# Performance work log

Hardware: AMD Instinct MI355X
Metric: run time of the kernel (lower is better)

## Reference

```python
import jax, jax.numpy as jnp
import numpy as np

C_IN = 12
C1 = 128
C2 = 256
K = 9
PAD = K // 2
T = 20
GAIN = 3.0
TAU1 = 1.0
TAU2 = 0.9
TH1 = 0.02
TH2 = 0.02
NUM_CLASSES = 4
B = 64
L = 2048


def _conv1d(x, w, b):
    # x: [B, Cin, L], w: [Cout, Cin, K] -> [B, Cout, L] (same padding)
    y = jax.lax.conv_general_dilated(
        x, w, window_strides=(1,), padding=[(PAD, PAD)],
        dimension_numbers=('NCH', 'OIH', 'NCH'))
    return y + b[None, :, None]


def setup_inputs() -> dict:
    key = jax.random.key(0)
    ks = jax.random.split(key, 7)
    x = jax.random.normal(ks[0], (B, C_IN, L, T), dtype=jnp.float32)
    fan1 = C_IN * K
    fan2 = C1 * K
    W1 = jax.random.uniform(ks[1], (C1, C_IN, K), jnp.float32, -1, 1) / np.sqrt(fan1)
    b1 = jax.random.uniform(ks[2], (C1,), jnp.float32, -1, 1) / np.sqrt(fan1)
    W2 = jax.random.uniform(ks[3], (C2, C1, K), jnp.float32, -1, 1) / np.sqrt(fan2)
    b2 = jax.random.uniform(ks[4], (C2,), jnp.float32, -1, 1) / np.sqrt(fan2)
    Wfc = jax.random.uniform(ks[5], (NUM_CLASSES, C2), jnp.float32, -1, 1) / np.sqrt(C2)
    bfc = jax.random.uniform(ks[6], (NUM_CLASSES,), jnp.float32, -1, 1) / np.sqrt(C2)
    return {"x": x, "W1": W1, "b1": b1, "W2": W2, "b2": b2, "Wfc": Wfc, "bfc": bfc}


def _lif(v, a, tau, th):
    # v <- v + (a - v)/tau; spike = hard threshold; reset to 0 where spiked
    v = v + (a - v) / tau
    spike = (v >= th).astype(v.dtype)
    v = jnp.where(spike > 0, jnp.zeros_like(v), v)
    return v, spike


def reference(x, W1, b1, W2, b2, Wfc, bfc):
    xt_seq = jnp.moveaxis(x, 3, 0)  # [T, B, Cin, L]
    v1_0 = jnp.zeros((B, C1, L), x.dtype)
    v2_0 = jnp.zeros((B, C2, L), x.dtype)

    def step(carry, xt):
        v1, v2 = carry
        a1 = _conv1d(xt, W1, b1) * GAIN
        v1, s1 = _lif(v1, a1, TAU1, TH1)
        a2 = _conv1d(s1, W2, b2) * GAIN
        v2, s2 = _lif(v2, a2, TAU2, TH2)
        return (v1, v2), s2

    _, spikes = jax.lax.scan(step, (v1_0, v2_0), xt_seq)  # [T, B, C2, L]
    out = jnp.sum(spikes, axis=0) / float(T)  # [B, C2, L]
    pooled = jnp.mean(out, axis=-1)  # AdaptiveAvgPool1d(1) + squeeze -> [B, C2]
    return pooled @ Wfc.T + bfc  # [B, NUM_CLASSES]
```

## Files before the change

### kernel.cpp

```cpp
#include <hip/hip_runtime.h>
#include <hip/hip_bf16.h>


#define NB    64
#define NCIN  12
#define NC1   128
#define NC2   256
#define NT    20
#define NL    2048
#define GAINF 3.0f
#define THF   0.02f
#define W2SCALE 4310.0f

#define BROWS 264
#define BSZ   (BROWS * 128)

typedef __bf16 bf16x8 __attribute__((ext_vector_type(8)));
typedef float  f32x4  __attribute__((ext_vector_type(4)));
typedef int    i32x4  __attribute__((ext_vector_type(4)));

__device__ __forceinline__ unsigned short f2bf(float f) {
  __hip_bfloat16 h = __float2bfloat16(f);
  return __builtin_bit_cast(unsigned short, h);
}

__global__ void snn_wsetup_kernel(const float* __restrict__ W1, const float* __restrict__ W2,
                                  unsigned short* __restrict__ w1t, unsigned char* __restrict__ w2q,
                                  unsigned char* __restrict__ s1p) {
  int idx = blockIdx.x * 256 + threadIdx.x;
  if (idx < 9 * 256 * 128) {
    int c1 = idx & 127;
    int c2 = (idx >> 7) & 255;
    int k  = idx >> 15;
    int c2q = c2 >> 6, c2l = c2 & 63;
    int dst = k * 32768 + c2q * 8192 + (((c2l * 128 + c1)) ^ ((c2l & 7) << 4));
    int q = __float2int_rn(W2[((size_t)c2 * 128 + c1) * 9 + k] * W2SCALE);
    w2q[dst] = (unsigned char)(signed char)q;
  }
  if (idx < 128 * 128) {
    int c1 = idx >> 7, kd = idx & 127;
    float v = 0.f;
    if (kd < 108) {
      int cin = kd / 9, kk = kd - cin * 9;
      v = W1[((size_t)c1 * 12 + cin) * 9 + kk];
    }
    w1t[idx] = f2bf(v);
  }
  if (idx < NB * NT * 8) {
    int bt = idx >> 3, r8 = idx & 7;
    size_t row = (size_t)bt * 2056 + (r8 < 4 ? r8 : 2048 + r8);
    *(uint4*)(s1p + row * 16) = make_uint4(0u, 0u, 0u, 0u);
  }
}

__global__ __launch_bounds__(256, 2) void snn_conv1_kernel(
    const float* __restrict__ x, const float* __restrict__ b1,
    const unsigned short* __restrict__ w1t, unsigned char* __restrict__ s1p) {
  __shared__ alignas(16) unsigned short ldsB[128 * 128];
  __shared__ alignas(16) unsigned short ldsA[128 * 128];
  __shared__ float b1s[128];

  const int tid  = threadIdx.x;
  const int lane = tid & 63;
  const int wv   = tid >> 6;
  const int wm   = wv >> 1, wn = wv & 1;
  const int hi   = lane >> 4, lo = lane & 15;
  const int bid  = blockIdx.x;
  const int t    = bid % 20;
  const int r    = bid / 20;
  const int l0   = (r & 15) << 7;
  const int b    = r >> 4;

  {
    const uint4* gA = (const uint4*)w1t;
#pragma unroll
    for (int i = 0; i < 8; ++i) {
      int idx = tid + i * 256;
      unsigned off = (unsigned)idx * 16u;
      unsigned row = off >> 8;
      *(uint4*)((char*)ldsA + (off ^ ((row & 7u) << 4))) = gA[idx];
    }
  }
  if (tid < 128) b1s[tid] = b1[tid];

  for (int i = tid; i < 128 * 20; i += 256) {
    int n = i / 20, c = 108 + (i - n * 20);
    *(unsigned short*)((char*)ldsB + ((unsigned)(n * 256) + (((unsigned)c * 2u) ^ (((unsigned)n & 7u) << 4)))) = 0;
  }
  for (int e = tid; e < NCIN * 136; e += 256) {
    int cin = e / 136, i = e - cin * 136;
    int l = l0 - 4 + i;
    float xv = 0.f;
    if (l >= 0 && l < NL) xv = x[(((size_t)b * NCIN + cin) * NL + l) * NT + t];
    unsigned short hv = f2bf(xv);
    int kd0 = cin * 9;
#pragma unroll
    for (int k = 0; k < 9; ++k) {
      int n = i - k;
      if (n >= 0 && n < 128) {
        *(unsigned short*)((char*)ldsB + ((unsigned)(n * 256) + (((unsigned)(kd0 + k) * 2u) ^ (((unsigned)n & 7u) << 4)))) = hv;
      }
    }
  }
  __syncthreads();

  f32x4 acc[4][4];
#pragma unroll
  for (int mf = 0; mf < 4; ++mf)
#pragma unroll
    for (int nf = 0; nf < 4; ++nf) acc[mf][nf] = (f32x4){0.f, 0.f, 0.f, 0.f};

#pragma unroll
  for (int chunk = 0; chunk < 4; ++chunk) {
    const unsigned kd2 = (unsigned)(chunk * 32 + hi * 8) * 2u;
    bf16x8 af[4], bfr[4];
#pragma unroll
    for (int mf = 0; mf < 4; ++mf) {
      int rr = wm * 64 + mf * 16 + lo;
      af[mf] = *(const bf16x8*)((const char*)ldsA + ((unsigned)(rr * 256) + (kd2 ^ (((unsigned)rr & 7u) << 4))));
    }
#pragma unroll
    for (int nf = 0; nf < 4; ++nf) {
      int rr = wn * 64 + nf * 16 + lo;
      bfr[nf] = *(const bf16x8*)((const char*)ldsB + ((unsigned)(rr * 256) + (kd2 ^ (((unsigned)rr & 7u) << 4))));
    }
#pragma unroll
    for (int mf = 0; mf < 4; ++mf)
#pragma unroll
      for (int nf = 0; nf < 4; ++nf)
        acc[mf][nf] = __builtin_amdgcn_mfma_f32_16x16x32_bf16(af[mf], bfr[nf], acc[mf][nf], 0, 0, 0);
  }
  __syncthreads();

  unsigned char* ldsP = (unsigned char*)ldsB;
#pragma unroll
  for (int mf = 0; mf < 4; ++mf) {
    int c1b = wm * 64 + mf * 16 + hi * 4;
#pragma unroll
    for (int nf = 0; nf < 4; ++nf) {
      int lrow = wn * 64 + nf * 16 + lo;
      unsigned n4 = 0;
      n4 |= (GAINF * (acc[mf][nf][0] + b1s[c1b + 0]) >= THF) ? 1u : 0u;
      n4 |= (GAINF * (acc[mf][nf][1] + b1s[c1b + 1]) >= THF) ? 2u : 0u;
      n4 |= (GAINF * (acc[mf][nf][2] + b1s[c1b + 2]) >= THF) ? 4u : 0u;
      n4 |= (GAINF * (acc[mf][nf][3] + b1s[c1b + 3]) >= THF) ? 8u : 0u;
      unsigned p = (unsigned)__shfl_xor((int)n4, 16);
      if ((hi & 1) == 0) {
        ldsP[lrow * 16 + (wm * 8 + mf * 2 + (hi >> 1))] = (unsigned char)(n4 | (p << 4));
      }
    }
  }
  __syncthreads();

  if (tid < 128) {
    uint4 v = *(const uint4*)(ldsP + tid * 16);
    *(uint4*)(s1p + ((size_t)(b * 20 + t) * 2056 + 4 + l0 + tid) * 16) = v;
  }
}

__device__ __forceinline__ void expand_store(unsigned char* buf, int n, int h, uint2 bits) {
  unsigned swz = (unsigned)(n & 7) << 4;
  char* rowp = (char*)buf + n * 128;
#pragma unroll
  for (int q = 0; q < 4; ++q) {
    unsigned src = (q < 2) ? bits.x : bits.y;
    int sh = (q & 1) * 16;
    uint4 w;
    w.x = (((src >> (sh + 0)) & 15u) * 0x204081u) & 0x01010101u;
    w.y = (((src >> (sh + 4)) & 15u) * 0x204081u) & 0x01010101u;
    w.z = (((src >> (sh + 8)) & 15u) * 0x204081u) & 0x01010101u;
    w.w = (((src >> (sh + 12)) & 15u) * 0x204081u) & 0x01010101u;
    *(uint4*)(rowp + (((unsigned)(h * 64 + q * 16)) ^ swz)) = w;
  }
}

__global__ __attribute__((amdgpu_flat_work_group_size(512, 512), amdgpu_waves_per_eu(2, 2)))
void snn_conv2_kernel(const unsigned char* __restrict__ s1p, const unsigned char* __restrict__ w2q,
                      const float* __restrict__ b2, float* __restrict__ counts) {
  __shared__ alignas(16) unsigned char ldsW[9 * 8192];
  __shared__ alignas(16) unsigned char ldsBy[2 * BSZ];

  const int tid  = threadIdx.x;
  const int lane = tid & 63;
  const int wv   = tid >> 6;
  const int hi   = lane >> 4, lo = lane & 15;
  const int bid  = blockIdx.x;
  const int b    = bid >> 5;
  const int r5b  = bid & 31;
  const int c2q  = r5b >> 3;
  const int l0   = (r5b & 7) << 8;

#pragma unroll
  for (int tp = 0; tp < 9; ++tp) {
    __builtin_amdgcn_global_load_lds(
        (const __attribute__((address_space(1))) void*)(w2q + (size_t)tp * 32768 + (size_t)c2q * 8192 + wv * 1024 + lane * 16),
        (__attribute__((address_space(3))) void*)(ldsW + tp * 8192 + wv * 1024), 16, 0, 0);
  }

  float gb2[4][4];
#pragma unroll
  for (int mf = 0; mf < 4; ++mf)
#pragma unroll
    for (int j = 0; j < 4; ++j)
      gb2[mf][j] = GAINF * b2[c2q * 64 + mf * 16 + hi * 4 + j];

  f32x4 v2s[4][2];
  int cnt[4][4];
#pragma unroll
  for (int mf = 0; mf < 4; ++mf) {
#pragma unroll
    for (int nf = 0; nf < 2; ++nf) v2s[mf][nf] = (f32x4){0.f, 0.f, 0.f, 0.f};
#pragma unroll
    for (int j = 0; j < 4; ++j) cnt[mf][j] = 0;
  }

  uint2 pA, pB, pC = make_uint2(0u, 0u);
  {
    const unsigned char* spA = s1p + ((size_t)(b * 20 + 0) * 2056 + l0) * 16;
    const unsigned char* spB = s1p + ((size_t)(b * 20 + 1) * 2056 + l0) * 16;
    pA = *(const uint2*)(spA + (size_t)tid * 8);
    pB = (tid < 16) ? *(const uint2*)(spA + (size_t)(512 + tid) * 8)
                    : *(const uint2*)(spB + (size_t)(tid - 16) * 8);
    if (tid < 32) pC = *(const uint2*)(spB + (size_t)(496 + tid) * 8);
  }

  const float it2 = 1.0f / 0.9f;
  const float isc = GAINF / W2SCALE;

  for (int ts = 0; ts < 20; ts += 2) {
    expand_store(ldsBy, tid >> 1, tid & 1, pA);
    if (tid < 16) expand_store(ldsBy, 256 + (tid >> 1), tid & 1, pB);
    else          expand_store(ldsBy + BSZ, (tid - 16) >> 1, (tid - 16) & 1, pB);
    if (tid < 32) expand_store(ldsBy + BSZ, 248 + (tid >> 1), tid & 1, pC);
    __syncthreads();

    if (ts < 18) {
      const unsigned char* snA = s1p + ((size_t)(b * 20 + ts + 2) * 2056 + l0) * 16;
      const unsigned char* snB = s1p + ((size_t)(b * 20 + ts + 3) * 2056 + l0) * 16;
      pA = *(const uint2*)(snA + (size_t)tid * 8);
      pB = (tid < 16) ? *(const uint2*)(snA + (size_t)(512 + tid) * 8)
                      : *(const uint2*)(snB + (size_t)(tid - 16) * 8);
      if (tid < 32) pC = *(const uint2*)(snB + (size_t)(496 + tid) * 8);
    }

    i32x4 acc[4][2][2];
#pragma unroll
    for (int mf = 0; mf < 4; ++mf)
#pragma unroll
      for (int tt = 0; tt < 2; ++tt)
#pragma unroll
        for (int nf = 0; nf < 2; ++nf) acc[mf][tt][nf] = (i32x4){0, 0, 0, 0};

#pragma unroll
    for (int tap = 0; tap < 9; ++tap) {
#pragma unroll
      for (int chunk = 0; chunk < 2; ++chunk) {
        const unsigned ksl = (unsigned)(chunk * 64 + hi * 16);
        i32x4 af[4], bf[2][2];
#pragma unroll
        for (int mf = 0; mf < 4; ++mf) {
          int rr = mf * 16 + lo;
          unsigned off = (unsigned)(rr * 128) + (ksl ^ (((unsigned)rr & 7u) << 4));
          af[mf] = *(const i32x4*)(ldsW + tap * 8192 + off);
        }
#pragma unroll
        for (int nf = 0; nf < 2; ++nf) {
          int rs = wv * 32 + nf * 16 + lo + tap;
          unsigned off = (unsigned)(rs * 128) + (ksl ^ (((unsigned)rs & 7u) << 4));
          bf[0][nf] = *(const i32x4*)(ldsBy + off);
          bf[1][nf] = *(const i32x4*)(ldsBy + BSZ + off);
        }
#pragma unroll
        for (int mf = 0; mf < 4; ++mf)
#pragma unroll
          for (int tt = 0; tt < 2; ++tt)
#pragma unroll
            for (int nf = 0; nf < 2; ++nf)
              acc[mf][tt][nf] = __builtin_amdgcn_mfma_i32_16x16x64_i8(af[mf], bf[tt][nf], acc[mf][tt][nf], 0, 0, 0);
      }
    }

#pragma unroll
    for (int tt = 0; tt < 2; ++tt) {
#pragma unroll
      for (int mf = 0; mf < 4; ++mf) {
#pragma unroll
        for (int nf = 0; nf < 2; ++nf) {
#pragma unroll
          for (int j = 0; j < 4; ++j) {
            float a2 = (float)acc[mf][tt][nf][j] * isc + gb2[mf][j];
            float vo = v2s[mf][nf][j];
            float vn = vo + (a2 - vo) * it2;
            int sp2 = (vn >= THF) ? 1 : 0;
            v2s[mf][nf][j] = sp2 ? 0.f : vn;
            cnt[mf][j] += sp2;
          }
        }
      }
    }

    __syncthreads();
  }

#pragma unroll
  for (int mf = 0; mf < 4; ++mf)
#pragma unroll
    for (int j = 0; j < 4; ++j) {
      int c = cnt[mf][j];
      c += __shfl_xor(c, 1);
      c += __shfl_xor(c, 2);
      c += __shfl_xor(c, 4);
      c += __shfl_xor(c, 8);
      if (lo == 0) {
        int c2g = c2q * 64 + mf * 16 + hi * 4 + j;
        atomicAdd(&counts[b * NC2 + c2g], (float)c);
      }
    }
}

__global__ void snn_fc_kernel(const float* __restrict__ counts, const float* __restrict__ Wfc,
                              const float* __restrict__ bfc, float* __restrict__ out) {
  int tid = threadIdx.x;
  int b = tid >> 2, cls = tid & 3;
  float s = 0.f;
  for (int c = 0; c < 256; ++c) s += counts[b * 256 + c] * Wfc[cls * 256 + c];
  out[tid] = s * (1.0f / ((float)NT * (float)NL)) + bfc[cls];
}

extern "C" void kernel_launch(void* const* d_in, const int* in_sizes, int n_in,
                              void* d_out, int out_size, void* d_ws, size_t ws_size,
                              hipStream_t stream) {
  const float* x   = (const float*)d_in[0];
  const float* W1  = (const float*)d_in[1];
  const float* b1  = (const float*)d_in[2];
  const float* W2  = (const float*)d_in[3];
  const float* b2  = (const float*)d_in[4];
  const float* Wfc = (const float*)d_in[5];
  const float* bfc = (const float*)d_in[6];
  float* out = (float*)d_out;
  char* ws = (char*)d_ws;

  const size_t SZ_S1P = (size_t)NB * NT * 2056 * 16;
  const size_t SZ_W2Q = (size_t)9 * 256 * 128;
  const size_t SZ_W1T = (size_t)128 * 128 * 2;
  const size_t SZ_CNT = (size_t)NB * NC2 * 4;

  const size_t OFF_S1P = 0;
  const size_t OFF_W2Q = OFF_S1P + SZ_S1P;
  const size_t OFF_W1T = OFF_W2Q + SZ_W2Q;
  const size_t OFF_CNT = OFF_W1T + SZ_W1T;
  const size_t NEEDED  = OFF_CNT + SZ_CNT;
  if (ws_size < NEEDED) return;

  unsigned char*  s1p = (unsigned char*)(ws + OFF_S1P);
  unsigned char*  w2q = (unsigned char*)(ws + OFF_W2Q);
  unsigned short* w1t = (unsigned short*)(ws + OFF_W1T);
  float* counts = (float*)(ws + OFF_CNT);

  hipMemsetAsync(counts, 0, SZ_CNT, stream);
  snn_wsetup_kernel<<<1152, 256, 0, stream>>>(W1, W2, w1t, w2q, s1p);
  snn_conv1_kernel<<<NB * 16 * NT, 256, 0, stream>>>(x, b1, w1t, s1p);
  snn_conv2_kernel<<<NB * 4 * 8, 512, 0, stream>>>(s1p, w2q, b2, counts);
  snn_fc_kernel<<<1, 256, 0, stream>>>(counts, Wfc, bfc, out);
}
```

Before: 930.5 us.

## Stream conv2 weights from global in MFMA fragment layout, process four timesteps per tile

Conv2 no longer stages the int8 W2 into LDS. Weights are pre-packed into MFMA A-fragment order and read straight from global/L2 into registers, double-buffered across k-slices. The freed LDS holds four timesteps of expanded spikes for a 128-position tile instead of two timesteps of 256, so each weight fragment is reused over four timesteps and the grid doubles. The cost is repeated global weight loads per block per iteration, which rely on cache hits, plus extra index arithmetic for the staged spike rows.

```diff
diff --git a/kernel.cpp b/kernel.cpp
--- a/kernel.cpp
+++ b/kernel.cpp
@@ -12,8 +12,8 @@
 #define THF   0.02f
 #define W2SCALE 4310.0f
 
-#define BROWS 264
-#define BSZ   (BROWS * 128)
+#define BROWS4 136
+#define BSZ4   (BROWS4 * 128)
 
 typedef __bf16 bf16x8 __attribute__((ext_vector_type(8)));
 typedef float  f32x4  __attribute__((ext_vector_type(4)));
@@ -25,17 +25,19 @@
 }
 
 __global__ void snn_wsetup_kernel(const float* __restrict__ W1, const float* __restrict__ W2,
-                                  unsigned short* __restrict__ w1t, unsigned char* __restrict__ w2q,
+                                  unsigned short* __restrict__ w1t, unsigned char* __restrict__ w2a,
                                   unsigned char* __restrict__ s1p) {
   int idx = blockIdx.x * 256 + threadIdx.x;
   if (idx < 9 * 256 * 128) {
     int c1 = idx & 127;
     int c2 = (idx >> 7) & 255;
     int k  = idx >> 15;
-    int c2q = c2 >> 6, c2l = c2 & 63;
-    int dst = k * 32768 + c2q * 8192 + (((c2l * 128 + c1)) ^ ((c2l & 7) << 4));
+    int c2q = c2 >> 6, rr = c2 & 63;
+    int mf = rr >> 4, lo = rr & 15;
+    int chunk = c1 >> 6, hi = (c1 >> 4) & 3, bb = c1 & 15;
+    int frag = ((c2q * 9 + k) * 2 + chunk) * 4 + mf;
     int q = __float2int_rn(W2[((size_t)c2 * 128 + c1) * 9 + k] * W2SCALE);
-    w2q[dst] = (unsigned char)(signed char)q;
+    w2a[(size_t)frag * 1024 + (hi * 16 + lo) * 16 + bb] = (unsigned char)(signed char)q;
   }
   if (idx < 128 * 128) {
     int c1 = idx >> 7, kd = idx & 127;
@@ -175,27 +177,21 @@
 }
 
 __global__ __attribute__((amdgpu_flat_work_group_size(512, 512), amdgpu_waves_per_eu(2, 2)))
-void snn_conv2_kernel(const unsigned char* __restrict__ s1p, const unsigned char* __restrict__ w2q,
+void snn_conv2_kernel(const unsigned char* __restrict__ s1p, const unsigned char* __restrict__ w2a,
                       const float* __restrict__ b2, float* __restrict__ counts) {
-  __shared__ alignas(16) unsigned char ldsW[9 * 8192];
-  __shared__ alignas(16) unsigned char ldsBy[2 * BSZ];
+  __shared__ alignas(16) unsigned char ldsBy[4 * BSZ4];
 
   const int tid  = threadIdx.x;
   const int lane = tid & 63;
   const int wv   = tid >> 6;
   const int hi   = lane >> 4, lo = lane & 15;
+  const int wl   = wv * 16;
   const int bid  = blockIdx.x;
-  const int b    = bid >> 5;
-  const int r5b  = bid & 31;
-  const int c2q  = r5b >> 3;
-  const int l0   = (r5b & 7) << 8;
-
-#pragma unroll
-  for (int tp = 0; tp < 9; ++tp) {
-    __builtin_amdgcn_global_load_lds(
-        (const __attribute__((address_space(1))) void*)(w2q + (size_t)tp * 32768 + (size_t)c2q * 8192 + wv * 1024 + lane * 16),
-        (__attribute__((address_space(3))) void*)(ldsW + tp * 8192 + wv * 1024), 16, 0, 0);
-  }
+  const int b    = bid >> 6;
+  const int c2q  = (bid >> 4) & 3;
+  const int l0   = (bid & 15) << 7;
+
+  const i32x4* wfrag = (const i32x4*)(w2a + (size_t)c2q * 9 * 2 * 4 * 1024);
 
   float gb2[4][4];
 #pragma unroll
@@ -204,97 +200,102 @@
     for (int j = 0; j < 4; ++j)
       gb2[mf][j] = GAINF * b2[c2q * 64 + mf * 16 + hi * 4 + j];
 
-  f32x4 v2s[4][2];
+  f32x4 v2s[4];
   int cnt[4][4];
 #pragma unroll
   for (int mf = 0; mf < 4; ++mf) {
-#pragma unroll
-    for (int nf = 0; nf < 2; ++nf) v2s[mf][nf] = (f32x4){0.f, 0.f, 0.f, 0.f};
+    v2s[mf] = (f32x4){0.f, 0.f, 0.f, 0.f};
 #pragma unroll
     for (int j = 0; j < 4; ++j) cnt[mf][j] = 0;
   }
 
   uint2 pA, pB, pC = make_uint2(0u, 0u);
   {
-    const unsigned char* spA = s1p + ((size_t)(b * 20 + 0) * 2056 + l0) * 16;
-    const unsigned char* spB = s1p + ((size_t)(b * 20 + 1) * 2056 + l0) * 16;
-    pA = *(const uint2*)(spA + (size_t)tid * 8);
-    pB = (tid < 16) ? *(const uint2*)(spA + (size_t)(512 + tid) * 8)
-                    : *(const uint2*)(spB + (size_t)(tid - 16) * 8);
-    if (tid < 32) pC = *(const uint2*)(spB + (size_t)(496 + tid) * 8);
+    int uA = tid;            int tA = uA / 272, rA = uA - tA * 272;
+    int uB = 512 + tid;      int tB = uB / 272, rB = uB - tB * 272;
+    pA = *(const uint2*)(s1p + ((size_t)(b * 20 + tA) * 2056 + l0 + (rA >> 1)) * 16 + (rA & 1) * 8);
+    pB = *(const uint2*)(s1p + ((size_t)(b * 20 + tB) * 2056 + l0 + (rB >> 1)) * 16 + (rB & 1) * 8);
+    if (tid < 64) {
+      int uC = 1024 + tid;   int tC = uC / 272, rC = uC - tC * 272;
+      pC = *(const uint2*)(s1p + ((size_t)(b * 20 + tC) * 2056 + l0 + (rC >> 1)) * 16 + (rC & 1) * 8);
+    }
   }
 
   const float it2 = 1.0f / 0.9f;
   const float isc = GAINF / W2SCALE;
 
-  for (int ts = 0; ts < 20; ts += 2) {
-    expand_store(ldsBy, tid >> 1, tid & 1, pA);
-    if (tid < 16) expand_store(ldsBy, 256 + (tid >> 1), tid & 1, pB);
-    else          expand_store(ldsBy + BSZ, (tid - 16) >> 1, (tid - 16) & 1, pB);
-    if (tid < 32) expand_store(ldsBy + BSZ, 248 + (tid >> 1), tid & 1, pC);
+  for (int ts = 0; ts < 20; ts += 4) {
+    {
+      int uA = tid;          int tA = uA / 272, rA = uA - tA * 272;
+      int uB = 512 + tid;    int tB = uB / 272, rB = uB - tB * 272;
+      expand_store(ldsBy + tA * BSZ4, rA >> 1, rA & 1, pA);
+      expand_store(ldsBy + tB * BSZ4, rB >> 1, rB & 1, pB);
+      if (tid < 64) {
+        int uC = 1024 + tid; int tC = uC / 272, rC = uC - tC * 272;
+        expand_store(ldsBy + tC * BSZ4, rC >> 1, rC & 1, pC);
+      }
+    }
     __syncthreads();
 
-    if (ts < 18) {
-      const unsigned char* snA = s1p + ((size_t)(b * 20 + ts + 2) * 2056 + l0) * 16;
-      const unsigned char* snB = s1p + ((size_t)(b * 20 + ts + 3) * 2056 + l0) * 16;
-      pA = *(const uint2*)(snA + (size_t)tid * 8);
-      pB = (tid < 16) ? *(const uint2*)(snA + (size_t)(512 + tid) * 8)
-                      : *(const uint2*)(snB + (size_t)(tid - 16) * 8);
-      if (tid < 32) pC = *(const uint2*)(snB + (size_t)(496 + tid) * 8);
-    }
-
-    i32x4 acc[4][2][2];
+    if (ts < 16) {
+      int tsn = ts + 4;
+      int uA = tid;          int tA = uA / 272, rA = uA - tA * 272;
+      int uB = 512 + tid;    int tB = uB / 272, rB = uB - tB * 272;
+      pA = *(const uint2*)(s1p + ((size_t)(b * 20 + tsn + tA) * 2056 + l0 + (rA >> 1)) * 16 + (rA & 1) * 8);
+      pB = *(const uint2*)(s1p + ((size_t)(b * 20 + tsn + tB) * 2056 + l0 + (rB >> 1)) * 16 + (rB & 1) * 8);
+      if (tid < 64) {
+        int uC = 1024 + tid; int tC = uC / 272, rC = uC - tC * 272;
+        pC = *(const uint2*)(s1p + ((size_t)(b * 20 + tsn + tC) * 2056 + l0 + (rC >> 1)) * 16 + (rC & 1) * 8);
+      }
+    }
+
+    i32x4 acc[4][4];
 #pragma unroll
     for (int mf = 0; mf < 4; ++mf)
 #pragma unroll
-      for (int tt = 0; tt < 2; ++tt)
-#pragma unroll
-        for (int nf = 0; nf < 2; ++nf) acc[mf][tt][nf] = (i32x4){0, 0, 0, 0};
-
-#pragma unroll
-    for (int tap = 0; tap < 9; ++tap) {
-#pragma unroll
-      for (int chunk = 0; chunk < 2; ++chunk) {
-        const unsigned ksl = (unsigned)(chunk * 64 + hi * 16);
-        i32x4 af[4], bf[2][2];
-#pragma unroll
-        for (int mf = 0; mf < 4; ++mf) {
-          int rr = mf * 16 + lo;
-          unsigned off = (unsigned)(rr * 128) + (ksl ^ (((unsigned)rr & 7u) << 4));
-          af[mf] = *(const i32x4*)(ldsW + tap * 8192 + off);
-        }
-#pragma unroll
-        for (int nf = 0; nf < 2; ++nf) {
-          int rs = wv * 32 + nf * 16 + lo + tap;
-          unsigned off = (unsigned)(rs * 128) + (ksl ^ (((unsigned)rs & 7u) << 4));
-          bf[0][nf] = *(const i32x4*)(ldsBy + off);
-          bf[1][nf] = *(const i32x4*)(ldsBy + BSZ + off);
-        }
+      for (int tt = 0; tt < 4; ++tt) acc[mf][tt] = (i32x4){0, 0, 0, 0};
+
+    i32x4 afb[2][4];
+#pragma unroll
+    for (int s0 = 0; s0 < 2; ++s0)
+#pragma unroll
+      for (int mf = 0; mf < 4; ++mf)
+        afb[s0][mf] = wfrag[(s0 * 4 + mf) * 64 + lane];
+
+#pragma unroll
+    for (int s = 0; s < 18; ++s) {
+      const int tap = s >> 1;
+      const unsigned ksl = (unsigned)((s & 1) * 64 + hi * 16);
+      const int rs = wl + lo + tap;
+      const unsigned off = (unsigned)(rs * 128) + (ksl ^ (((unsigned)rs & 7u) << 4));
+      i32x4 bfr[4];
+#pragma unroll
+      for (int tt = 0; tt < 4; ++tt)
+        bfr[tt] = *(const i32x4*)(ldsBy + tt * BSZ4 + off);
+#pragma unroll
+      for (int mf = 0; mf < 4; ++mf)
+#pragma unroll
+        for (int tt = 0; tt < 4; ++tt)
+          acc[mf][tt] = __builtin_amdgcn_mfma_i32_16x16x64_i8(afb[s & 1][mf], bfr[tt], acc[mf][tt], 0, 0, 0);
+      if (s < 16) {
 #pragma unroll
         for (int mf = 0; mf < 4; ++mf)
-#pragma unroll
-          for (int tt = 0; tt < 2; ++tt)
-#pragma unroll
-            for (int nf = 0; nf < 2; ++nf)
-              acc[mf][tt][nf] = __builtin_amdgcn_mfma_i32_16x16x64_i8(af[mf], bf[tt][nf], acc[mf][tt][nf], 0, 0, 0);
-      }
-    }
-
-#pragma unroll
-    for (int tt = 0; tt < 2; ++tt) {
+          afb[s & 1][mf] = wfrag[((s + 2) * 4 + mf) * 64 + lane];
+      }
+    }
+
+#pragma unroll
+    for (int tt = 0; tt < 4; ++tt) {
 #pragma unroll
       for (int mf = 0; mf < 4; ++mf) {
 #pragma unroll
-        for (int nf = 0; nf < 2; ++nf) {
-#pragma unroll
-          for (int j = 0; j < 4; ++j) {
-            float a2 = (float)acc[mf][tt][nf][j] * isc + gb2[mf][j];
-            float vo = v2s[mf][nf][j];
-            float vn = vo + (a2 - vo) * it2;
-            int sp2 = (vn >= THF) ? 1 : 0;
-            v2s[mf][nf][j] = sp2 ? 0.f : vn;
-            cnt[mf][j] += sp2;
-          }
+        for (int j = 0; j < 4; ++j) {
+          float a2 = (float)acc[mf][tt][j] * isc + gb2[mf][j];
+          float vo = v2s[mf][j];
+          float vn = vo + (a2 - vo) * it2;
+          int sp2 = (vn >= THF) ? 1 : 0;
+          v2s[mf][j] = sp2 ? 0.f : vn;
+          cnt[mf][j] += sp2;
         }
       }
     }
@@ -341,25 +342,25 @@
   char* ws = (char*)d_ws;
 
   const size_t SZ_S1P = (size_t)NB * NT * 2056 * 16;
-  const size_t SZ_W2Q = (size_t)9 * 256 * 128;
+  const size_t SZ_W2A = (size_t)9 * 256 * 128;
   const size_t SZ_W1T = (size_t)128 * 128 * 2;
   const size_t SZ_CNT = (size_t)NB * NC2 * 4;
 
   const size_t OFF_S1P = 0;
-  const size_t OFF_W2Q = OFF_S1P + SZ_S1P;
-  const size_t OFF_W1T = OFF_W2Q + SZ_W2Q;
+  const size_t OFF_W2A = OFF_S1P + SZ_S1P;
+  const size_t OFF_W1T = OFF_W2A + SZ_W2A;
   const size_t OFF_CNT = OFF_W1T + SZ_W1T;
   const size_t NEEDED  = OFF_CNT + SZ_CNT;
   if (ws_size < NEEDED) return;
 
   unsigned char*  s1p = (unsigned char*)(ws + OFF_S1P);
-  unsigned char*  w2q = (unsigned char*)(ws + OFF_W2Q);
+  unsigned char*  w2a = (unsigned char*)(ws + OFF_W2A);
   unsigned short* w1t = (unsigned short*)(ws + OFF_W1T);
   float* counts = (float*)(ws + OFF_CNT);
 
   hipMemsetAsync(counts, 0, SZ_CNT, stream);
-  snn_wsetup_kernel<<<1152, 256, 0, stream>>>(W1, W2, w1t, w2q, s1p);
+  snn_wsetup_kernel<<<1152, 256, 0, stream>>>(W1, W2, w1t, w2a, s1p);
   snn_conv1_kernel<<<NB * 16 * NT, 256, 0, stream>>>(x, b1, w1t, s1p);
-  snn_conv2_kernel<<<NB * 4 * 8, 512, 0, stream>>>(s1p, w2q, b2, counts);
+  snn_conv2_kernel<<<NB * 4 * 16, 512, 0, stream>>>(s1p, w2a, b2, counts);
   snn_fc_kernel<<<1, 256, 0, stream>>>(counts, Wfc, bfc, out);
 }
```

Result: slower. 2.422 ms (+160.3%).

## Halve conv2 tile length and stream W2 taps through double-buffered LDS

Applied to the files above, without the earlier changes.

The conv2 kernel tile shrinks from 256 to 128 positions per block, and the grid doubles. Instead of keeping all nine W2 tap slices resident in LDS, it double-buffers one tap at a time with async global-to-LDS loads. This cuts LDS use from about 140KB to about 50KB and halves the accumulator registers, so more waves per EU can be resident (waves_per_eu 4) to hide latency. The cost is a barrier after every tap, W2 being re-read from global nine times per timestep pair, and more halo rows relative to the tile size.

```diff
diff --git a/kernel.cpp b/kernel.cpp
--- a/kernel.cpp
+++ b/kernel.cpp
@@ -12,8 +12,8 @@
 #define THF   0.02f
 #define W2SCALE 4310.0f
 
-#define BROWS 264
-#define BSZ   (BROWS * 128)
+#define BROWS2 136
+#define BSZ2   (BROWS2 * 128)
 
 typedef __bf16 bf16x8 __attribute__((ext_vector_type(8)));
 typedef float  f32x4  __attribute__((ext_vector_type(4)));
@@ -174,28 +174,20 @@
   }
 }
 
-__global__ __attribute__((amdgpu_flat_work_group_size(512, 512), amdgpu_waves_per_eu(2, 2)))
+__global__ __attribute__((amdgpu_flat_work_group_size(512, 512), amdgpu_waves_per_eu(4)))
 void snn_conv2_kernel(const unsigned char* __restrict__ s1p, const unsigned char* __restrict__ w2q,
                       const float* __restrict__ b2, float* __restrict__ counts) {
-  __shared__ alignas(16) unsigned char ldsW[9 * 8192];
-  __shared__ alignas(16) unsigned char ldsBy[2 * BSZ];
+  __shared__ alignas(16) unsigned char ldsW[2 * 8192];
+  __shared__ alignas(16) unsigned char ldsBy[2 * BSZ2];
 
   const int tid  = threadIdx.x;
   const int lane = tid & 63;
   const int wv   = tid >> 6;
   const int hi   = lane >> 4, lo = lane & 15;
   const int bid  = blockIdx.x;
-  const int b    = bid >> 5;
-  const int r5b  = bid & 31;
-  const int c2q  = r5b >> 3;
-  const int l0   = (r5b & 7) << 8;
-
-#pragma unroll
-  for (int tp = 0; tp < 9; ++tp) {
-    __builtin_amdgcn_global_load_lds(
-        (const __attribute__((address_space(1))) void*)(w2q + (size_t)tp * 32768 + (size_t)c2q * 8192 + wv * 1024 + lane * 16),
-        (__attribute__((address_space(3))) void*)(ldsW + tp * 8192 + wv * 1024), 16, 0, 0);
-  }
+  const int b    = bid >> 6;
+  const int c2q  = (bid >> 4) & 3;
+  const int l0   = (bid & 15) << 7;
 
   float gb2[4][4];
 #pragma unroll
@@ -204,80 +196,90 @@
     for (int j = 0; j < 4; ++j)
       gb2[mf][j] = GAINF * b2[c2q * 64 + mf * 16 + hi * 4 + j];
 
-  f32x4 v2s[4][2];
+  f32x4 v2s[4];
   int cnt[4][4];
 #pragma unroll
   for (int mf = 0; mf < 4; ++mf) {
-#pragma unroll
-    for (int nf = 0; nf < 2; ++nf) v2s[mf][nf] = (f32x4){0.f, 0.f, 0.f, 0.f};
+    v2s[mf] = (f32x4){0.f, 0.f, 0.f, 0.f};
 #pragma unroll
     for (int j = 0; j < 4; ++j) cnt[mf][j] = 0;
   }
 
-  uint2 pA, pB, pC = make_uint2(0u, 0u);
+  uint2 pA, pB = make_uint2(0u, 0u);
   {
-    const unsigned char* spA = s1p + ((size_t)(b * 20 + 0) * 2056 + l0) * 16;
-    const unsigned char* spB = s1p + ((size_t)(b * 20 + 1) * 2056 + l0) * 16;
-    pA = *(const uint2*)(spA + (size_t)tid * 8);
-    pB = (tid < 16) ? *(const uint2*)(spA + (size_t)(512 + tid) * 8)
-                    : *(const uint2*)(spB + (size_t)(tid - 16) * 8);
-    if (tid < 32) pC = *(const uint2*)(spB + (size_t)(496 + tid) * 8);
-  }
+    pA = *(const uint2*)(s1p + ((size_t)(b * 20 + (tid >= 272)) * 2056 + l0 +
+                                ((tid >= 272 ? tid - 272 : tid) >> 1)) * 16 + (tid & 1) * 8);
+    if (tid < 32) {
+      int u = 512 + tid;
+      pB = *(const uint2*)(s1p + ((size_t)(b * 20 + 1) * 2056 + l0 + ((u - 272) >> 1)) * 16 + (u & 1) * 8);
+    }
+  }
+
+  __builtin_amdgcn_global_load_lds(
+      (const __attribute__((address_space(1))) void*)(w2q + (size_t)c2q * 8192 + wv * 1024 + lane * 16),
+      (__attribute__((address_space(3))) void*)(ldsW + wv * 1024), 16, 0, 0);
+  int cur = 0;
 
   const float it2 = 1.0f / 0.9f;
   const float isc = GAINF / W2SCALE;
 
   for (int ts = 0; ts < 20; ts += 2) {
-    expand_store(ldsBy, tid >> 1, tid & 1, pA);
-    if (tid < 16) expand_store(ldsBy, 256 + (tid >> 1), tid & 1, pB);
-    else          expand_store(ldsBy + BSZ, (tid - 16) >> 1, (tid - 16) & 1, pB);
-    if (tid < 32) expand_store(ldsBy + BSZ, 248 + (tid >> 1), tid & 1, pC);
+    {
+      int tt = (tid >= 272), r = tid - 272 * tt;
+      expand_store(ldsBy + tt * BSZ2, r >> 1, tid & 1, pA);
+      if (tid < 32) expand_store(ldsBy + BSZ2, (512 + tid - 272) >> 1, tid & 1, pB);
+    }
     __syncthreads();
 
     if (ts < 18) {
-      const unsigned char* snA = s1p + ((size_t)(b * 20 + ts + 2) * 2056 + l0) * 16;
-      const unsigned char* snB = s1p + ((size_t)(b * 20 + ts + 3) * 2056 + l0) * 16;
-      pA = *(const uint2*)(snA + (size_t)tid * 8);
-      pB = (tid < 16) ? *(const uint2*)(snA + (size_t)(512 + tid) * 8)
-                      : *(const uint2*)(snB + (size_t)(tid - 16) * 8);
-      if (tid < 32) pC = *(const uint2*)(snB + (size_t)(496 + tid) * 8);
-    }
-
-    i32x4 acc[4][2][2];
+      pA = *(const uint2*)(s1p + ((size_t)(b * 20 + ts + 2 + (tid >= 272)) * 2056 + l0 +
+                                  ((tid >= 272 ? tid - 272 : tid) >> 1)) * 16 + (tid & 1) * 8);
+      if (tid < 32) {
+        int u = 512 + tid;
+        pB = *(const uint2*)(s1p + ((size_t)(b * 20 + ts + 3) * 2056 + l0 + ((u - 272) >> 1)) * 16 + (u & 1) * 8);
+      }
+    }
+
+    i32x4 acc[4][2];
 #pragma unroll
     for (int mf = 0; mf < 4; ++mf)
 #pragma unroll
-      for (int tt = 0; tt < 2; ++tt)
-#pragma unroll
-        for (int nf = 0; nf < 2; ++nf) acc[mf][tt][nf] = (i32x4){0, 0, 0, 0};
+      for (int tt = 0; tt < 2; ++tt) acc[mf][tt] = (i32x4){0, 0, 0, 0};
 
 #pragma unroll
     for (int tap = 0; tap < 9; ++tap) {
+      {
+        int tapn = (tap == 8) ? 0 : tap + 1;
+        __builtin_amdgcn_global_load_lds(
+            (const __attribute__((address_space(1))) void*)(w2q + (size_t)tapn * 32768 + (size_t)c2q * 8192 + wv * 1024 + lane * 16),
+            (__attribute__((address_space(3))) void*)(ldsW + ((cur ^ 1) << 13) + wv * 1024), 16, 0, 0);
+      }
+      const unsigned char* wbuf = ldsW + (cur << 13);
+      __builtin_amdgcn_s_setprio(1);
 #pragma unroll
       for (int chunk = 0; chunk < 2; ++chunk) {
         const unsigned ksl = (unsigned)(chunk * 64 + hi * 16);
-        i32x4 af[4], bf[2][2];
+        i32x4 af[4], bfr[2];
 #pragma unroll
         for (int mf = 0; mf < 4; ++mf) {
           int rr = mf * 16 + lo;
-          unsigned off = (unsigned)(rr * 128) + (ksl ^ (((unsigned)rr & 7u) << 4));
-          af[mf] = *(const i32x4*)(ldsW + tap * 8192 + off);
+          af[mf] = *(const i32x4*)(wbuf + (unsigned)(rr * 128) + (ksl ^ (((unsigned)rr & 7u) << 4)));
         }
-#pragma unroll
-        for (int nf = 0; nf < 2; ++nf) {
-          int rs = wv * 32 + nf * 16 + lo + tap;
+        {
+          int rs = wv * 16 + lo + tap;
           unsigned off = (unsigned)(rs * 128) + (ksl ^ (((unsigned)rs & 7u) << 4));
-          bf[0][nf] = *(const i32x4*)(ldsBy + off);
-          bf[1][nf] = *(const i32x4*)(ldsBy + BSZ + off);
+          bfr[0] = *(const i32x4*)(ldsBy + off);
+          bfr[1] = *(const i32x4*)(ldsBy + BSZ2 + off);
         }
 #pragma unroll
         for (int mf = 0; mf < 4; ++mf)
 #pragma unroll
           for (int tt = 0; tt < 2; ++tt)
-#pragma unroll
-            for (int nf = 0; nf < 2; ++nf)
-              acc[mf][tt][nf] = __builtin_amdgcn_mfma_i32_16x16x64_i8(af[mf], bf[tt][nf], acc[mf][tt][nf], 0, 0, 0);
-      }
+            acc[mf][tt] = __builtin_amdgcn_mfma_i32_16x16x64_i8(af[mf], bfr[tt], acc[mf][tt], 0, 0, 0);
+      }
+      __builtin_amdgcn_s_setprio(0);
+      __syncthreads();
+      cur ^= 1;
     }
 
 #pragma unroll
@@ -285,21 +287,16 @@
 #pragma unroll
       for (int mf = 0; mf < 4; ++mf) {
 #pragma unroll
-        for (int nf = 0; nf < 2; ++nf) {
-#pragma unroll
-          for (int j = 0; j < 4; ++j) {
-            float a2 = (float)acc[mf][tt][nf][j] * isc + gb2[mf][j];
-            float vo = v2s[mf][nf][j];
-            float vn = vo + (a2 - vo) * it2;
-            int sp2 = (vn >= THF) ? 1 : 0;
-            v2s[mf][nf][j] = sp2 ? 0.f : vn;
-            cnt[mf][j] += sp2;
-          }
+        for (int j = 0; j < 4; ++j) {
+          float a2 = (float)acc[mf][tt][j] * isc + gb2[mf][j];
+          float vo = v2s[mf][j];
+          float vn = vo + (a2 - vo) * it2;
+          int sp2 = (vn >= THF) ? 1 : 0;
+          v2s[mf][j] = sp2 ? 0.f : vn;
+          cnt[mf][j] += sp2;
         }
       }
     }
-
-    __syncthreads();
   }
 
 #pragma unroll
@@ -360,6 +357,6 @@
   hipMemsetAsync(counts, 0, SZ_CNT, stream);
   snn_wsetup_kernel<<<1152, 256, 0, stream>>>(W1, W2, w1t, w2q, s1p);
   snn_conv1_kernel<<<NB * 16 * NT, 256, 0, stream>>>(x, b1, w1t, s1p);
-  snn_conv2_kernel<<<NB * 4 * 8, 512, 0, stream>>>(s1p, w2q, b2, counts);
+  snn_conv2_kernel<<<NB * 4 * 16, 512, 0, stream>>>(s1p, w2q, b2, counts);
   snn_fc_kernel<<<1, 256, 0, stream>>>(counts, Wfc, bfc, out);
 }
```

Result: slower. 1.503 ms (+61.5%).

## Process four timesteps per conv1 block with vectorized x loads

Applied to the files above, without the earlier changes.

Each conv1 block now covers four consecutive timesteps, loading x as float4 along the contiguous T axis into a staged LDS buffer. It then loops over the timesteps to rebuild the im2col tile and run the MFMA GEMM. This replaces strided scalar global reads and amortizes the W1 and bias LDS setup across timesteps. In exchange, LDS use per block rises and per-block work grows while the grid shrinks fivefold, which may reduce occupancy.

```diff
diff --git a/kernel.cpp b/kernel.cpp
--- a/kernel.cpp
+++ b/kernel.cpp
@@ -58,6 +58,8 @@
     const unsigned short* __restrict__ w1t, unsigned char* __restrict__ s1p) {
   __shared__ alignas(16) unsigned short ldsB[128 * 128];
   __shared__ alignas(16) unsigned short ldsA[128 * 128];
+  __shared__ alignas(16) unsigned short xt[NCIN * 136 * 4];
+  __shared__ alignas(16) unsigned char  ldsP[128 * 16];
   __shared__ float b1s[128];
 
   const int tid  = threadIdx.x;
@@ -66,8 +68,8 @@
   const int wm   = wv >> 1, wn = wv & 1;
   const int hi   = lane >> 4, lo = lane & 15;
   const int bid  = blockIdx.x;
-  const int t    = bid % 20;
-  const int r    = bid / 20;
+  const int tg   = bid % 5;
+  const int r    = bid / 5;
   const int l0   = (r & 15) << 7;
   const int b    = r >> 4;
 
@@ -87,74 +89,93 @@
     int n = i / 20, c = 108 + (i - n * 20);
     *(unsigned short*)((char*)ldsB + ((unsigned)(n * 256) + (((unsigned)c * 2u) ^ (((unsigned)n & 7u) << 4)))) = 0;
   }
-  for (int e = tid; e < NCIN * 136; e += 256) {
-    int cin = e / 136, i = e - cin * 136;
-    int l = l0 - 4 + i;
-    float xv = 0.f;
-    if (l >= 0 && l < NL) xv = x[(((size_t)b * NCIN + cin) * NL + l) * NT + t];
-    unsigned short hv = f2bf(xv);
-    int kd0 = cin * 9;
-#pragma unroll
-    for (int k = 0; k < 9; ++k) {
-      int n = i - k;
-      if (n >= 0 && n < 128) {
-        *(unsigned short*)((char*)ldsB + ((unsigned)(n * 256) + (((unsigned)(kd0 + k) * 2u) ^ (((unsigned)n & 7u) << 4)))) = hv;
-      }
+
+#pragma unroll
+  for (int k = 0; k < 7; ++k) {
+    int u = tid + k * 256;
+    if (u < NCIN * 136) {
+      int cin = u / 136, ll = u - cin * 136;
+      int l = l0 - 4 + ll;
+      float4 f = make_float4(0.f, 0.f, 0.f, 0.f);
+      if (l >= 0 && l < NL)
+        f = *(const float4*)(x + (((size_t)b * NCIN + cin) * NL + l) * NT + tg * 4);
+      uint2 w;
+      w.x = (unsigned)f2bf(f.x) | ((unsigned)f2bf(f.y) << 16);
+      w.y = (unsigned)f2bf(f.z) | ((unsigned)f2bf(f.w) << 16);
+      *(uint2*)&xt[u * 4] = w;
     }
   }
   __syncthreads();
 
-  f32x4 acc[4][4];
-#pragma unroll
-  for (int mf = 0; mf < 4; ++mf)
-#pragma unroll
-    for (int nf = 0; nf < 4; ++nf) acc[mf][nf] = (f32x4){0.f, 0.f, 0.f, 0.f};
-
-#pragma unroll
-  for (int chunk = 0; chunk < 4; ++chunk) {
-    const unsigned kd2 = (unsigned)(chunk * 32 + hi * 8) * 2u;
-    bf16x8 af[4], bfr[4];
+  for (int tt = 0; tt < 4; ++tt) {
+#pragma unroll
+    for (int k = 0; k < 7; ++k) {
+      int e = tid + k * 256;
+      if (e < NCIN * 136) {
+        int cin = e / 136, i = e - cin * 136;
+        unsigned short hv = xt[e * 4 + tt];
+        int kd0 = cin * 9;
+#pragma unroll
+        for (int kk = 0; kk < 9; ++kk) {
+          int n = i - kk;
+          if (n >= 0 && n < 128) {
+            *(unsigned short*)((char*)ldsB + ((unsigned)(n * 256) + (((unsigned)(kd0 + kk) * 2u) ^ (((unsigned)n & 7u) << 4)))) = hv;
+          }
+        }
+      }
+    }
+    __syncthreads();
+
+    f32x4 acc[4][4];
+#pragma unroll
+    for (int mf = 0; mf < 4; ++mf)
+#pragma unroll
+      for (int nf = 0; nf < 4; ++nf) acc[mf][nf] = (f32x4){0.f, 0.f, 0.f, 0.f};
+
+#pragma unroll
+    for (int chunk = 0; chunk < 4; ++chunk) {
+      const unsigned kd2 = (unsigned)(chunk * 32 + hi * 8) * 2u;
+      bf16x8 af[4], bfr[4];
+#pragma unroll
+      for (int mf = 0; mf < 4; ++mf) {
+        int rr = wm * 64 + mf * 16 + lo;
+        af[mf] = *(const bf16x8*)((const char*)ldsA + ((unsigned)(rr * 256) + (kd2 ^ (((unsigned)rr & 7u) << 4))));
+      }
+#pragma unroll
+      for (int nf = 0; nf < 4; ++nf) {
+        int rr = wn * 64 + nf * 16 + lo;
+        bfr[nf] = *(const bf16x8*)((const char*)ldsB + ((unsigned)(rr * 256) + (kd2 ^ (((unsigned)rr & 7u) << 4))));
+      }
+#pragma unroll
+      for (int mf = 0; mf < 4; ++mf)
+#pragma unroll
+        for (int nf = 0; nf < 4; ++nf)
+          acc[mf][nf] = __builtin_amdgcn_mfma_f32_16x16x32_bf16(af[mf], bfr[nf], acc[mf][nf], 0, 0, 0);
+    }
+
 #pragma unroll
     for (int mf = 0; mf < 4; ++mf) {
-      int rr = wm * 64 + mf * 16 + lo;
-      af[mf] = *(const bf16x8*)((const char*)ldsA + ((unsigned)(rr * 256) + (kd2 ^ (((unsigned)rr & 7u) << 4))));
-    }
-#pragma unroll
-    for (int nf = 0; nf < 4; ++nf) {
-      int rr = wn * 64 + nf * 16 + lo;
-      bfr[nf] = *(const bf16x8*)((const char*)ldsB + ((unsigned)(rr * 256) + (kd2 ^ (((unsigned)rr & 7u) << 4))));
-    }
-#pragma unroll
-    for (int mf = 0; mf < 4; ++mf)
-#pragma unroll
-      for (int nf = 0; nf < 4; ++nf)
-        acc[mf][nf] = __builtin_amdgcn_mfma_f32_16x16x32_bf16(af[mf], bfr[nf], acc[mf][nf], 0, 0, 0);
-  }
-  __syncthreads();
-
-  unsigned char* ldsP = (unsigned char*)ldsB;
-#pragma unroll
-  for (int mf = 0; mf < 4; ++mf) {
-    int c1b = wm * 64 + mf * 16 + hi * 4;
-#pragma unroll
-    for (int nf = 0; nf < 4; ++nf) {
-      int lrow = wn * 64 + nf * 16 + lo;
-      unsigned n4 = 0;
-      n4 |= (GAINF * (acc[mf][nf][0] + b1s[c1b + 0]) >= THF) ? 1u : 0u;
-      n4 |= (GAINF * (acc[mf][nf][1] + b1s[c1b + 1]) >= THF) ? 2u : 0u;
-      n4 |= (GAINF * (acc[mf][nf][2] + b1s[c1b + 2]) >= THF) ? 4u : 0u;
-      n4 |= (GAINF * (acc[mf][nf][3] + b1s[c1b + 3]) >= THF) ? 8u : 0u;
-      unsigned p = (unsigned)__shfl_xor((int)n4, 16);
-      if ((hi & 1) == 0) {
-        ldsP[lrow * 16 + (wm * 8 + mf * 2 + (hi >> 1))] = (unsigned char)(n4 | (p << 4));
-      }
-    }
-  }
-  __syncthreads();
-
-  if (tid < 128) {
-    uint4 v = *(const uint4*)(ldsP + tid * 16);
-    *(uint4*)(s1p + ((size_t)(b * 20 + t) * 2056 + 4 + l0 + tid) * 16) = v;
+      int c1b = wm * 64 + mf * 16 + hi * 4;
+#pragma unroll
+      for (int nf = 0; nf < 4; ++nf) {
+        int lrow = wn * 64 + nf * 16 + lo;
+        unsigned n4 = 0;
+        n4 |= (GAINF * (acc[mf][nf][0] + b1s[c1b + 0]) >= THF) ? 1u : 0u;
+        n4 |= (GAINF * (acc[mf][nf][1] + b1s[c1b + 1]) >= THF) ? 2u : 0u;
+        n4 |= (GAINF * (acc[mf][nf][2] + b1s[c1b + 2]) >= THF) ? 4u : 0u;
+        n4 |= (GAINF * (acc[mf][nf][3] + b1s[c1b + 3]) >= THF) ? 8u : 0u;
+        unsigned p = (unsigned)__shfl_xor((int)n4, 16);
+        if ((hi & 1) == 0) {
+          ldsP[lrow * 16 + (wm * 8 + mf * 2 + (hi >> 1))] = (unsigned char)(n4 | (p << 4));
+        }
+      }
+    }
+    __syncthreads();
+
+    if (tid < 128) {
+      uint4 v = *(const uint4*)(ldsP + tid * 16);
+      *(uint4*)(s1p + ((size_t)(b * 20 + tg * 4 + tt) * 2056 + 4 + l0 + tid) * 16) = v;
+    }
   }
 }
 
@@ -359,7 +380,7 @@
 
   hipMemsetAsync(counts, 0, SZ_CNT, stream);
   snn_wsetup_kernel<<<1152, 256, 0, stream>>>(W1, W2, w1t, w2q, s1p);
-  snn_conv1_kernel<<<NB * 16 * NT, 256, 0, stream>>>(x, b1, w1t, s1p);
+  snn_conv1_kernel<<<NB * 16 * 5, 256, 0, stream>>>(x, b1, w1t, s1p);
   snn_conv2_kernel<<<NB * 4 * 8, 512, 0, stream>>>(s1p, w2q, b2, counts);
   snn_fc_kernel<<<1, 256, 0, stream>>>(counts, Wfc, bfc, out);
 }
```

Measured after the change: 836.0 us (median of 2 runs). 1.11x faster.
